# Performance work log

Measured on AMD Instinct MI355X. Metric: run time of the kernel, lower is better.

Reference implementation:

```python
import jax, jax.numpy as jnp
import numpy as np

H = 2048          # n_hidden
TUNED = 10        # n_hidden_tuned (hardcoded in module)
B, T = 16, 1024
NIN, NOUT = 8, 8
TAU = 0.01
TAU_FACIL = 1.5
P_REL = 1.0
BETA = 1.5 * P_REL
DT = 0.001
PROB_C = 0.1


def setup_inputs() -> dict:
    key = jax.random.key(0)
    ks = jax.random.split(key, 8)
    w_in_std = 1.0 / np.sqrt(H)
    w_h_std = 1.6 / np.sqrt(PROB_C * H)
    return {
        "x": jax.random.normal(ks[0], (B, T, NIN), jnp.float32),
        "h_0": jax.random.normal(ks[1], (B, H), jnp.float32),
        "W_ih": jax.random.normal(ks[2], (H, NIN), jnp.float32) * w_in_std,
        "W_hh_tuned": jax.random.normal(ks[3], (H, TUNED), jnp.float32) * w_h_std,
        "W_hh_fixed": jax.random.normal(ks[4], (H, H - TUNED), jnp.float32) * w_h_std,
        "W_hh_mask": (jax.random.uniform(ks[5], (H, H)) < PROB_C).astype(jnp.float32),
        "W_hz": jax.random.normal(ks[6], (NOUT, H), jnp.float32) * (1.0 / np.sqrt(H)),
        "W_zh": jnp.zeros((H, NOUT), jnp.float32),  # echo_state=False -> zeros
        "tau_depr": jax.random.uniform(ks[7], (H,), minval=0.05, maxval=1.0),
    }


def reference(x, h_0, W_ih, W_hh_tuned, W_hh_fixed, W_hh_mask, W_hz, W_zh, tau_depr):
    # masked recurrent weight: mask * concat(tuned, fixed) along columns
    Wm = W_hh_mask * jnp.concatenate([W_hh_tuned, W_hh_fixed], axis=1)  # [H,H]

    def step(carry, x_t):
        h, r, u, hT = carry                       # each [B,H]; hT = tanh(h)
        z_prev = hT @ W_hz.T                      # [B,NOUT], z_{t-1}
        r_t = r + ((P_REL - r) / tau_depr - BETA * r * hT) * DT
        u_t = u + ((P_REL - u) / TAU_FACIL + BETA * (1.0 - u) * hT) * DT
        # presyn_scaling = r_{t-1}; noise_std = 0 so noise term drops out
        dh = (-h + (r * hT) @ Wm.T + x_t @ W_ih.T + z_prev @ W_zh.T) / TAU
        h_t = h + dh * DT
        hT_t = jnp.tanh(h_t)
        z_t = hT_t @ W_hz.T
        return (h_t, r_t, u_t, hT_t), (z_t, h_t, r_t)

    init = (h_0, jnp.full_like(h_0, P_REL), jnp.full_like(h_0, P_REL), jnp.tanh(h_0))
    _, (z, h, r) = jax.lax.scan(step, init, jnp.swapaxes(x, 0, 1))  # time-major scan
    return jnp.swapaxes(z, 0, 1), jnp.swapaxes(h, 0, 1), jnp.swapaxes(r, 0, 1)
```

## Files before the change

### kernel.cpp

```cpp
#include <hip/hip_runtime.h>

#define HDIM   2048
#define TUNEDC 10
#define BATCH  16
#define TSTEPS 1024
#define NINP   8
#define NOUTP  8
#define RPW    8
#define NWG    (HDIM / RPW)
#define NTHR   256

#define DT_C   0.001f
#define TAU_C  0.01f
#define PREL_C 1.0f
#define BETA_C 1.5f

#define NCTR      16
#define CTRSTRIDE 32
#define VBUF_OFF  1024
#define VBUF_SZ   (BATCH * HDIM)

#define SCR_STRIDE 140
#define LDS_YH     (128 * SCR_STRIDE)
#define LDS_TOTAL  (LDS_YH + 256)

#define AGENT __HIP_MEMORY_SCOPE_AGENT

extern "C" __global__ __launch_bounds__(NTHR, 1)
void rnn_main(const float* __restrict__ x, const float* __restrict__ h0,
              const float* __restrict__ Wih, const float* __restrict__ Wt,
              const float* __restrict__ Wf, const float* __restrict__ Wmask,
              const float* __restrict__ tau_d,
              float* __restrict__ h_out, float* __restrict__ r_out,
              int* ctr, float* vbuf)
{
    extern __shared__ float smem[];
    float* scr = smem;
    float* yh  = smem + LDS_YH;

    const int wg   = blockIdx.x;
    const int tid  = threadIdx.x;
    const int lane = tid & 63;
    const int w    = tid >> 6;
    const int bg   = w & 1;
    const int kh   = w >> 1;
    const int r0   = wg * RPW;
    int* myctr = ctr + (wg & (NCTR - 1)) * CTRSTRIDE;

    float wreg[RPW][16];
    #pragma unroll
    for (int rl = 0; rl < RPW; ++rl) {
        const int r = r0 + rl;
        const float* mrow = Wmask + (size_t)r * HDIM;
        #pragma unroll
        for (int jj = 0; jj < 16; ++jj) {
            int k = kh * 1024 + jj * 64 + lane;
            float base = (k < TUNEDC) ? Wt[r * TUNEDC + k]
                                      : Wf[r * (HDIM - TUNEDC) + (k - TUNEDC)];
            wreg[rl][jj] = mrow[k] * base;
        }
    }

    const bool owner = (tid < BATCH * RPW);
    const int ob  = tid >> 3;
    const int orl = tid & 7;
    const int oro = r0 + orl;
    float h_s = 0.f, r_s = PREL_C, hT_s = 0.f, itau_s = 1.f;
    float wihr[NINP];
    if (owner) {
        h_s   = h0[ob * HDIM + oro];
        hT_s  = tanhf(h_s);
        itau_s = 1.0f / tau_d[oro];
        #pragma unroll
        for (int k2 = 0; k2 < NINP; ++k2) wihr[k2] = Wih[oro * NINP + k2];
        __hip_atomic_store(&vbuf[ob * HDIM + oro], r_s * hT_s,
                           __ATOMIC_RELAXED, AGENT);
    }
    __builtin_amdgcn_fence(__ATOMIC_RELEASE, "workgroup");
    __syncthreads();
    if (tid == 0)
        __hip_atomic_fetch_add(myctr, 1, __ATOMIC_RELAXED, AGENT);

    for (int t = 0; t < TSTEPS; ++t) {
        if (w == 0) {
            const int target = NCTR * (t + 1);
            while (true) {
                int cv = 0x7fffffff;
                if (lane < NCTR)
                    cv = __hip_atomic_load(&ctr[lane * CTRSTRIDE],
                                           __ATOMIC_RELAXED, AGENT);
                if (__all(cv >= target)) break;
                __builtin_amdgcn_s_sleep(1);
            }
        }
        __syncthreads();

        const float* vc = vbuf + (t & 1) * VBUF_SZ;

        float acc[RPW][8];
        #pragma unroll
        for (int rl = 0; rl < RPW; ++rl)
            #pragma unroll
            for (int bl = 0; bl < 8; ++bl) acc[rl][bl] = 0.f;

        #pragma unroll
        for (int jj = 0; jj < 16; ++jj) {
            const int k = kh * 1024 + jj * 64 + lane;
            float vv[8];
            #pragma unroll
            for (int bl = 0; bl < 8; ++bl)
                vv[bl] = __hip_atomic_load(&vc[(8 * bg + bl) * HDIM + k],
                                           __ATOMIC_RELAXED, AGENT);
            #pragma unroll
            for (int rl = 0; rl < RPW; ++rl) {
                float wv = wreg[rl][jj];
                #pragma unroll
                for (int bl = 0; bl < 8; ++bl)
                    acc[rl][bl] = fmaf(wv, vv[bl], acc[rl][bl]);
            }
        }

        {
            const int ks = kh * 64 + lane;
            #pragma unroll
            for (int rl = 0; rl < RPW; ++rl)
                #pragma unroll
                for (int bl = 0; bl < 8; ++bl) {
                    int p = (8 * bg + bl) * 8 + rl;
                    scr[p * SCR_STRIDE + ks] = acc[rl][bl];
                }
        }
        __syncthreads();
        {
            const int p  = tid & 127;
            const int hh = tid >> 7;
            const float4* s4 = (const float4*)(scr + p * SCR_STRIDE + hh * 64);
            float s = 0.f;
            #pragma unroll
            for (int i = 0; i < 16; ++i) {
                float4 q = s4[i];
                s += q.x + q.y + q.z + q.w;
            }
            yh[p * 2 + hh] = s;
        }
        __syncthreads();

        float hn = 0.f, rn = 0.f;
        if (owner) {
            float y = yh[tid * 2] + yh[tid * 2 + 1];
            const float* xt = x + ((size_t)ob * TSTEPS + t) * NINP;
            float xin = 0.f;
            #pragma unroll
            for (int k2 = 0; k2 < NINP; ++k2)
                xin = fmaf(xt[k2], wihr[k2], xin);
            float dh = (y + xin - h_s) * (1.0f / TAU_C);
            hn = fmaf(dh, DT_C, h_s);
            rn = r_s + ((PREL_C - r_s) * itau_s - BETA_C * r_s * hT_s) * DT_C;
            float hTn = tanhf(hn);
            h_s = hn; r_s = rn; hT_s = hTn;
            if (t + 1 < TSTEPS) {
                float* vn = vbuf + ((t + 1) & 1) * VBUF_SZ;
                __hip_atomic_store(&vn[ob * HDIM + oro], r_s * hT_s,
                                   __ATOMIC_RELAXED, AGENT);
            }
        }
        if (t + 1 < TSTEPS) {
            __builtin_amdgcn_fence(__ATOMIC_RELEASE, "workgroup");
            __syncthreads();
            if (tid == 0)
                __hip_atomic_fetch_add(myctr, 1, __ATOMIC_RELAXED, AGENT);
        }
        if (owner) {
            size_t oidx = ((size_t)ob * TSTEPS + t) * HDIM + oro;
            h_out[oidx] = hn;
            r_out[oidx] = rn;
        }
    }
}

extern "C" __global__ __launch_bounds__(256, 2)
void z_kernel(const float* __restrict__ h_out, const float* __restrict__ Whz,
              float* __restrict__ z_out)
{
    const int bt  = blockIdx.x;
    const int tid = threadIdx.x;
    const float4* hp = (const float4*)(h_out + (size_t)bt * HDIM);
    float4 a = hp[tid * 2], b4 = hp[tid * 2 + 1];
    float th[8] = { tanhf(a.x),  tanhf(a.y),  tanhf(a.z),  tanhf(a.w),
                    tanhf(b4.x), tanhf(b4.y), tanhf(b4.z), tanhf(b4.w) };
    float acc[NOUTP];
    #pragma unroll
    for (int o = 0; o < NOUTP; ++o) {
        const float4* wp = (const float4*)(Whz + o * HDIM);
        float4 wa = wp[tid * 2], wb = wp[tid * 2 + 1];
        acc[o] = th[0]*wa.x + th[1]*wa.y + th[2]*wa.z + th[3]*wa.w
               + th[4]*wb.x + th[5]*wb.y + th[6]*wb.z + th[7]*wb.w;
    }
    #pragma unroll
    for (int off = 32; off > 0; off >>= 1)
        #pragma unroll
        for (int o = 0; o < NOUTP; ++o)
            acc[o] += __shfl_down(acc[o], off, 64);
    __shared__ float part[4][NOUTP];
    if ((tid & 63) == 0)
        for (int o = 0; o < NOUTP; ++o) part[tid >> 6][o] = acc[o];
    __syncthreads();
    if (tid < NOUTP)
        z_out[(size_t)bt * NOUTP + tid] =
            part[0][tid] + part[1][tid] + part[2][tid] + part[3][tid];
}

extern "C" void kernel_launch(void* const* d_in, const int* in_sizes, int n_in,
                              void* d_out, int out_size, void* d_ws, size_t ws_size,
                              hipStream_t stream)
{
    (void)in_sizes; (void)n_in; (void)out_size; (void)ws_size;
    const float* x    = (const float*)d_in[0];
    const float* h0   = (const float*)d_in[1];
    const float* Wih  = (const float*)d_in[2];
    const float* Wt   = (const float*)d_in[3];
    const float* Wf   = (const float*)d_in[4];
    const float* Wm   = (const float*)d_in[5];
    const float* Whz  = (const float*)d_in[6];
    const float* taud = (const float*)d_in[8];

    float* z_out = (float*)d_out;
    float* h_out = z_out + (size_t)BATCH * TSTEPS * NOUTP;
    float* r_out = h_out + (size_t)BATCH * TSTEPS * HDIM;

    int*   ctr  = (int*)d_ws;
    float* vbuf = (float*)d_ws + VBUF_OFF;

    hipFuncSetAttribute((const void*)rnn_main,
                        hipFuncAttributeMaxDynamicSharedMemorySize,
                        LDS_TOTAL * (int)sizeof(float));

    hipMemsetAsync(ctr, 0, VBUF_OFF * sizeof(int), stream);
    rnn_main<<<NWG, NTHR, LDS_TOTAL * sizeof(float), stream>>>(
        x, h0, Wih, Wt, Wf, Wm, taud, h_out, r_out, ctr, vbuf);
    z_kernel<<<BATCH * TSTEPS, 256, 0, stream>>>(h_out, Whz, z_out);
}
```

Measured before the change: 6.786 ms.

## Double rows per workgroup and stage the shared state vector through LDS

Each workgroup now handles 16 rows with 512 threads, so there are half as many workgroups taking part in the grid-wide step barrier. The previous-step vector is loaded from global memory once per workgroup with 64-bit atomic loads into a double-buffered LDS tile, prefetched two chunks ahead, and the two row halves read it from LDS instead of each fetching it from global. The counter target is adjusted for the new workgroup count. In exchange it adds a block barrier per chunk inside the inner loop, and the launch bound of two blocks per CU may limit registers and cause spills of the 128-float weight array.

```diff
diff --git a/kernel.cpp b/kernel.cpp
--- a/kernel.cpp
+++ b/kernel.cpp
@@ -6,9 +6,9 @@
 #define TSTEPS 1024
 #define NINP   8
 #define NOUTP  8
-#define RPW    8
+#define RPW    16
 #define NWG    (HDIM / RPW)
-#define NTHR   256
+#define NTHR   512
 
 #define DT_C   0.001f
 #define TAU_C  0.01f
@@ -20,13 +20,17 @@
 #define VBUF_OFF  1024
 #define VBUF_SZ   (BATCH * HDIM)
 
-#define SCR_STRIDE 140
-#define LDS_YH     (128 * SCR_STRIDE)
-#define LDS_TOTAL  (LDS_YH + 256)
+#define LDS_V      0
+#define SCR_STRIDE 132
+#define LDS_SCR    4096
+#define LDS_YH     (LDS_SCR + 256 * SCR_STRIDE)
+#define LDS_TOTAL  (LDS_YH + 512)
 
 #define AGENT __HIP_MEMORY_SCOPE_AGENT
 
-extern "C" __global__ __launch_bounds__(NTHR, 1)
+typedef unsigned long long ull;
+
+extern "C" __global__ __launch_bounds__(NTHR, 2)
 void rnn_main(const float* __restrict__ x, const float* __restrict__ h0,
               const float* __restrict__ Wih, const float* __restrict__ Wt,
               const float* __restrict__ Wf, const float* __restrict__ Wmask,
@@ -35,22 +39,29 @@
               int* ctr, float* vbuf)
 {
     extern __shared__ float smem[];
-    float* scr = smem;
-    float* yh  = smem + LDS_YH;
+    float* ldsv = smem + LDS_V;
+    float* scr  = smem + LDS_SCR;
+    float* yh   = smem + LDS_YH;
 
     const int wg   = blockIdx.x;
     const int tid  = threadIdx.x;
     const int lane = tid & 63;
     const int w    = tid >> 6;
     const int bg   = w & 1;
-    const int kh   = w >> 1;
+    const int kh   = (w >> 1) & 1;
+    const int rh   = w >> 2;
     const int r0   = wg * RPW;
     int* myctr = ctr + (wg & (NCTR - 1)) * CTRSTRIDE;
 
-    float wreg[RPW][16];
+    const int sflat = tid * 4;
+    const int sb    = sflat >> 7;
+    const int skh   = (sflat >> 6) & 1;
+    const int su    = sflat & 63;
+
+    float wreg[8][16];
     #pragma unroll
-    for (int rl = 0; rl < RPW; ++rl) {
-        const int r = r0 + rl;
+    for (int rl = 0; rl < 8; ++rl) {
+        const int r = r0 + rh * 8 + rl;
         const float* mrow = Wmask + (size_t)r * HDIM;
         #pragma unroll
         for (int jj = 0; jj < 16; ++jj) {
@@ -62,8 +73,8 @@
     }
 
     const bool owner = (tid < BATCH * RPW);
-    const int ob  = tid >> 3;
-    const int orl = tid & 7;
+    const int ob  = tid >> 4;
+    const int orl = tid & 15;
     const int oro = r0 + orl;
     float h_s = 0.f, r_s = PREL_C, hT_s = 0.f, itau_s = 1.f;
     float wihr[NINP];
@@ -83,7 +94,7 @@
 
     for (int t = 0; t < TSTEPS; ++t) {
         if (w == 0) {
-            const int target = NCTR * (t + 1);
+            const int target = (NWG / NCTR) * (t + 1);
             while (true) {
                 int cv = 0x7fffffff;
                 if (lane < NCTR)
@@ -96,44 +107,69 @@
         __syncthreads();
 
         const float* vc = vbuf + (t & 1) * VBUF_SZ;
-
-        float acc[RPW][8];
-        #pragma unroll
-        for (int rl = 0; rl < RPW; ++rl)
+        const float* sbase = vc + sb * HDIM + skh * 1024 + su;
+
+        ull ca = __hip_atomic_load((const ull*)(sbase), __ATOMIC_RELAXED, AGENT);
+        ull cb = __hip_atomic_load((const ull*)(sbase) + 1, __ATOMIC_RELAXED, AGENT);
+        ull na = __hip_atomic_load((const ull*)(sbase + 64), __ATOMIC_RELAXED, AGENT);
+        ull nb = __hip_atomic_load((const ull*)(sbase + 64) + 1, __ATOMIC_RELAXED, AGENT);
+        {
+            union { ull u; float f[2]; } p0, p1; p0.u = ca; p1.u = cb;
+            float4 q = { p0.f[0], p0.f[1], p1.f[0], p1.f[1] };
+            *(float4*)&ldsv[sflat] = q;
+        }
+        __syncthreads();
+
+        float acc[8][8];
+        #pragma unroll
+        for (int rl = 0; rl < 8; ++rl)
             #pragma unroll
             for (int bl = 0; bl < 8; ++bl) acc[rl][bl] = 0.f;
 
         #pragma unroll
         for (int jj = 0; jj < 16; ++jj) {
-            const int k = kh * 1024 + jj * 64 + lane;
+            const int cur = jj & 1;
+            ull fa = 0, fb = 0;
+            if (jj + 2 < 16) {
+                fa = __hip_atomic_load((const ull*)(sbase + (jj + 2) * 64),
+                                       __ATOMIC_RELAXED, AGENT);
+                fb = __hip_atomic_load((const ull*)(sbase + (jj + 2) * 64) + 1,
+                                       __ATOMIC_RELAXED, AGENT);
+            }
             float vv[8];
             #pragma unroll
             for (int bl = 0; bl < 8; ++bl)
-                vv[bl] = __hip_atomic_load(&vc[(8 * bg + bl) * HDIM + k],
-                                           __ATOMIC_RELAXED, AGENT);
-            #pragma unroll
-            for (int rl = 0; rl < RPW; ++rl) {
+                vv[bl] = ldsv[cur * 2048 + (8 * bg + bl) * 128 + kh * 64 + lane];
+            #pragma unroll
+            for (int rl = 0; rl < 8; ++rl) {
                 float wv = wreg[rl][jj];
                 #pragma unroll
                 for (int bl = 0; bl < 8; ++bl)
                     acc[rl][bl] = fmaf(wv, vv[bl], acc[rl][bl]);
             }
+            if (jj + 1 < 16) {
+                union { ull u; float f[2]; } p0, p1; p0.u = na; p1.u = nb;
+                float4 q = { p0.f[0], p0.f[1], p1.f[0], p1.f[1] };
+                *(float4*)&ldsv[(cur ^ 1) * 2048 + sflat] = q;
+            }
+            na = fa; nb = fb;
+            if (jj + 1 < 16) __syncthreads();
         }
 
         {
             const int ks = kh * 64 + lane;
             #pragma unroll
-            for (int rl = 0; rl < RPW; ++rl)
+            for (int rl = 0; rl < 8; ++rl)
                 #pragma unroll
                 for (int bl = 0; bl < 8; ++bl) {
-                    int p = (8 * bg + bl) * 8 + rl;
+                    int p = (8 * bg + bl) * 16 + rh * 8 + rl;
                     scr[p * SCR_STRIDE + ks] = acc[rl][bl];
                 }
         }
         __syncthreads();
         {
-            const int p  = tid & 127;
-            const int hh = tid >> 7;
+            const int p  = tid & 255;
+            const int hh = tid >> 8;
             const float4* s4 = (const float4*)(scr + p * SCR_STRIDE + hh * 64);
             float s = 0.f;
             #pragma unroll
```

Result: slower. 7.586 ms (+11.8%).
